# Optimization experiments

Measured on AMD Instinct MI355X. Metric: run time of the kernel, lower is better.

## Reference

```python
import jax, jax.numpy as jnp
import numpy as np

EMBEDDING_DIM = 64
N_EMBEDDINGS = 512


def setup_inputs() -> dict:
    key = jax.random.key(0)
    k1, k2 = jax.random.split(key)
    inputs = jax.random.normal(k1, (32, 64, 64, 64), dtype=jnp.float32)  # NCHW, C==embedding_dim
    weight = jax.random.normal(k2, (N_EMBEDDINGS, EMBEDDING_DIM), dtype=jnp.float32)
    return {"inputs": inputs, "weight": weight}


def reference(inputs, weight):
    # NCHW -> NHWC, flatten to [N, D]
    x = jnp.transpose(inputs, (0, 2, 3, 1))  # [B, H, W, D]
    in_shape = x.shape
    flat = x.reshape(-1, EMBEDDING_DIM)  # [N, D]

    distances = (
        jnp.sum(flat * flat, axis=1, keepdims=True)
        + jnp.sum(weight * weight, axis=1)
        - 2.0 * flat @ weight.T
    )
    idx = jnp.argmin(distances, axis=1)  # [N]

    # one-hot @ weight is just a gather
    quantized = weight[idx].reshape(in_shape)  # [B, H, W, D]

    # commitment loss: mse(stop_grad(quantized), x)
    e_latent_loss = jnp.mean(jnp.square(jax.lax.stop_gradient(quantized) - x))

    # straight-through estimator
    quantized = x + jax.lax.stop_gradient(quantized - x)

    return jnp.transpose(quantized, (0, 3, 1, 2)), e_latent_loss
```

## Files before the change

### kernel.cpp

```cpp
#include <hip/hip_runtime.h>
#include <math.h>

typedef short bf16x8 __attribute__((ext_vector_type(8)));
typedef float f32x4 __attribute__((ext_vector_type(4)));

#define VQ_D 64
#define VQ_K 512
#define VQ_NQ 131072
#define VQ_TOTAL 8388608
#define NT 32
#define TAU 8e-3f

__device__ __forceinline__ ushort bf16_rne(float f) {
    uint u = __builtin_bit_cast(uint, f);
    u += 0x7fffu + ((u >> 16) & 1u);
    return (ushort)(u >> 16);
}
__device__ __forceinline__ float bf16_to_f(ushort h) {
    uint u = ((uint)h) << 16;
    return __builtin_bit_cast(float, u);
}

__global__ __launch_bounds__(128) void vq_prep(const float* __restrict__ w,
                                               ushort* __restrict__ wfrag,
                                               float* __restrict__ wn,
                                               float* __restrict__ out) {
    if (blockIdx.x == 0 && threadIdx.x == 0) out[VQ_TOTAL] = 0.f;
    const int k = blockIdx.x * 128 + threadIdx.x;
    const float4* row = (const float4*)(w + k * VQ_D);
    const int t = k >> 4, col = k & 15;
    float nrm = 0.f;
    for (int g = 0; g < 8; ++g) {
        float4 a = row[2 * g], b4 = row[2 * g + 1];
        float v[8] = {a.x, a.y, a.z, a.w, b4.x, b4.y, b4.z, b4.w};
        ushort hi[8], lo[8];
#pragma unroll
        for (int j = 0; j < 8; ++j) {
            nrm = fmaf(v[j], v[j], nrm);
            hi[j] = bf16_rne(v[j]);
            lo[j] = bf16_rne(v[j] - bf16_to_f(hi[j]));
        }
        const int quad = g & 3, fh = g >> 2;
        const int lane = quad * 16 + col;
        bf16x8* basez = (bf16x8*)wfrag + t * 256 + lane;
        *(basez + fh * 64)       = *(bf16x8*)hi;
        *(basez + (2 + fh) * 64) = *(bf16x8*)lo;
    }
    wn[k] = nrm;
}

__global__ __launch_bounds__(256, 3) void vq_main(const float* __restrict__ in,
                                                  const float* __restrict__ w,
                                                  const ushort* __restrict__ wfrag,
                                                  const float* __restrict__ wng,
                                                  float* __restrict__ out) {
    __shared__ float xn_lds[128];
    __shared__ float best_lds[128], sec_lds[128];
    __shared__ int   bi_lds[128], si_lds[128];

    const int tid  = threadIdx.x;
    const int lane = tid & 63;
    const int wid  = tid >> 6;
    const int col  = lane & 15;
    const int quad = lane >> 4;
    const int n0  = blockIdx.x * 128;
    const int b   = n0 >> 12;
    const int hw0 = n0 & 4095;
    const float* xg0 = in + (b << 18) + hw0;
    const float* xgW = xg0 + wid * 32;

    bf16x8 ah0[2], ah1[2], al0[2], al1[2];
#pragma unroll
    for (int T = 0; T < 2; ++T) {
        const float* xq = xgW + T * 16 + col;
        float sx = 0.f;
        ushort h0[8], l0[8], h1[8], l1[8];
#pragma unroll
        for (int j = 0; j < 8; ++j) {
            float v0 = xq[(quad * 8 + j) << 12];
            float v1 = xq[(32 + quad * 8 + j) << 12];
            sx = fmaf(v0, v0, sx);
            sx = fmaf(v1, v1, sx);
            h0[j] = bf16_rne(v0); l0[j] = bf16_rne(v0 - bf16_to_f(h0[j]));
            h1[j] = bf16_rne(v1); l1[j] = bf16_rne(v1 - bf16_to_f(h1[j]));
        }
        ah0[T] = *(bf16x8*)h0; al0[T] = *(bf16x8*)l0;
        ah1[T] = *(bf16x8*)h1; al1[T] = *(bf16x8*)l1;
        sx += __shfl_xor(sx, 16, 64);
        sx += __shfl_xor(sx, 32, 64);
        if (quad == 0) xn_lds[wid * 32 + T * 16 + col] = sx;
    }

    float best[8], sec[8];
#pragma unroll
    for (int r = 0; r < 8; ++r) { best[r] = 3.0e38f; sec[r] = 3.0e38f; }

    const bf16x8* wf = (const bf16x8*)wfrag + lane;
    bf16x8 bh0 = wf[0], bh1 = wf[64], bl0 = wf[128], bl1 = wf[192];
    float wnv = wng[col];

#pragma unroll 1
    for (int t = 0; t < NT; ++t) {
        bf16x8 nh0, nh1, nl0, nl1;
        float wnn;
        if (t + 1 < NT) {
            const bf16x8* nx = wf + (t + 1) * 256;
            nh0 = nx[0]; nh1 = nx[64]; nl0 = nx[128]; nl1 = nx[192];
            wnn = wng[(t + 1) * 16 + col];
        }
#pragma unroll
        for (int T = 0; T < 2; ++T) {
            f32x4 accP = {0.f, 0.f, 0.f, 0.f}, accQ = {0.f, 0.f, 0.f, 0.f};
            accP = __builtin_amdgcn_mfma_f32_16x16x32_bf16(ah0[T], bh0, accP, 0, 0, 0);
            accP = __builtin_amdgcn_mfma_f32_16x16x32_bf16(ah1[T], bh1, accP, 0, 0, 0);
            accQ = __builtin_amdgcn_mfma_f32_16x16x32_bf16(ah0[T], bl0, accQ, 0, 0, 0);
            accQ = __builtin_amdgcn_mfma_f32_16x16x32_bf16(ah1[T], bl1, accQ, 0, 0, 0);
            accQ = __builtin_amdgcn_mfma_f32_16x16x32_bf16(al0[T], bh0, accQ, 0, 0, 0);
            accQ = __builtin_amdgcn_mfma_f32_16x16x32_bf16(al1[T], bh1, accQ, 0, 0, 0);
#pragma unroll
            for (int j = 0; j < 4; ++j) {
                float dist = fmaf(-2.f, accP[j] + accQ[j], wnv);
                uint u = (__builtin_bit_cast(uint, dist) & 0xFFFFFFE0u) | (uint)t;
                float key = __builtin_bit_cast(float, u);
                const int r = T * 4 + j;
                float m = fmaxf(best[r], key);
                best[r] = fminf(best[r], key);
                sec[r]  = fminf(sec[r], m);
            }
        }
        bh0 = nh0; bh1 = nh1; bl0 = nl0; bl1 = nl1; wnv = wnn;
    }

    float bD[8], sD[8];
    int bI[8], sI[8];
#pragma unroll
    for (int r = 0; r < 8; ++r) {
        uint ub = __builtin_bit_cast(uint, best[r]);
        uint us = __builtin_bit_cast(uint, sec[r]);
        bI[r] = (int)(ub & 31u) * 16 + col;
        sI[r] = (int)(us & 31u) * 16 + col;
        bD[r] = __builtin_bit_cast(float, ub & 0xFFFFFFE0u);
        sD[r] = __builtin_bit_cast(float, us & 0xFFFFFFE0u);
    }

#pragma unroll
    for (int off = 1; off < 16; off <<= 1) {
#pragma unroll
        for (int r = 0; r < 8; ++r) {
            float ob = __shfl_xor(bD[r], off, 64);
            float os = __shfl_xor(sD[r], off, 64);
            int   oi = __shfl_xor(bI[r], off, 64);
            int   oc = __shfl_xor(sI[r], off, 64);
            bool oWins = (ob < bD[r]) || (ob == bD[r] && oi < bI[r]);
            float nb  = oWins ? ob    : bD[r];
            int   ni  = oWins ? oi    : bI[r];
            float c1  = oWins ? bD[r] : ob;
            int   ci1 = oWins ? bI[r] : oi;
            float c2  = oWins ? os    : sD[r];
            int   ci2 = oWins ? oc    : sI[r];
            bool c1w = (c1 < c2) || (c1 == c2 && ci1 < ci2);
            sD[r] = c1w ? c1  : c2;
            sI[r] = c1w ? ci1 : ci2;
            bD[r] = nb; bI[r] = ni;
        }
    }
    if (col == 0) {
#pragma unroll
        for (int r = 0; r < 8; ++r) {
            const int q = wid * 32 + (r >> 2) * 16 + quad * 4 + (r & 3);
            best_lds[q] = bD[r]; sec_lds[q] = sD[r];
            bi_lds[q] = bI[r];   si_lds[q] = sI[r];
        }
    }
    __syncthreads();

    if (tid < 128) {
        const int q = tid;
        float cb = best_lds[q], cs = sec_lds[q];
        int cbi = bi_lds[q], csi = si_lds[q];
        double chosen = (double)cb;
        if (cs - cb < TAU) {
            const float* wb  = w + cbi * VQ_D;
            const float* ws2 = w + csi * VQ_D;
            const float* xqp = xg0 + q;
            double nb = 0.0, dotb = 0.0, ns = 0.0, dots = 0.0;
            for (int d = 0; d < VQ_D; ++d) {
                double xv = (double)xqp[d << 12];
                double wbv = (double)wb[d], wsv = (double)ws2[d];
                nb = fma(wbv, wbv, nb); dotb = fma(xv, wbv, dotb);
                ns = fma(wsv, wsv, ns); dots = fma(xv, wsv, dots);
            }
            double db = nb - 2.0 * dotb, ds = ns - 2.0 * dots;
            if (ds < db || (ds == db && csi < cbi)) { cbi = csi; chosen = ds; }
            else                                    { chosen = db; }
        }
        bi_lds[q] = cbi;
        double lq = (double)xn_lds[q] + chosen;
#pragma unroll
        for (int off = 32; off > 0; off >>= 1)
            lq += __shfl_down(lq, off, 64);
        if ((tid & 63) == 0)
            atomicAdd(out + VQ_TOTAL, (float)(lq * (1.0 / (double)VQ_TOTAL)));
    }
    __syncthreads();

    {
        const int q = tid & 127, half = tid >> 7;
        const float4* wrow = (const float4*)(w + bi_lds[q] * VQ_D) + half * 8;
        float* op = out + (b << 18) + hw0 + q;
#pragma unroll
        for (int u = 0; u < 8; ++u) {
            float4 v = wrow[u];
            const int d = half * 32 + 4 * u;
            op[(d + 0) << 12] = v.x;
            op[(d + 1) << 12] = v.y;
            op[(d + 2) << 12] = v.z;
            op[(d + 3) << 12] = v.w;
        }
    }
}

extern "C" void kernel_launch(void* const* d_in, const int* in_sizes, int n_in,
                              void* d_out, int out_size, void* d_ws, size_t ws_size,
                              hipStream_t stream) {
    const float* in = (const float*)d_in[0];
    const float* w  = (const float*)d_in[1];
    float* out = (float*)d_out;

    ushort* wfrag = (ushort*)d_ws;
    float*  wn    = (float*)((char*)d_ws + 131072);

    vq_prep<<<4, 128, 0, stream>>>(w, wfrag, wn, out);
    vq_main<<<VQ_NQ / 128, 256, 0, stream>>>(in, w, wfrag, wn, out);
}
```

Before: 139.7 us.

## Split codebook across two waves per 32-query block and merge top-2 in LDS

Each block now handles 32 queries with two waves, each scanning half of the codebook (16 tiles), and the two waves' best and second-best candidates are merged through LDS. The MFMA accumulators are merged into a single chain and the software prefetch of the next weight tile is removed. The aim is more blocks and waves for latency hiding and a shorter per-wave loop. In exchange, each input column is loaded twice (once per wave), atomics per query block rise fourfold, and the MFMA chain becomes serial with no prefetch.

After: 179.7 us. 1.29x slower.

```diff
diff --git a/kernel.cpp b/kernel.cpp
--- a/kernel.cpp
+++ b/kernel.cpp
@@ -8,7 +8,7 @@
 #define VQ_K 512
 #define VQ_NQ 131072
 #define VQ_TOTAL 8388608
-#define NT 32
+#define NTH 16
 #define TAU 8e-3f
 
 __device__ __forceinline__ ushort bf16_rne(float f) {
@@ -49,30 +49,29 @@
     wn[k] = nrm;
 }
 
-__global__ __launch_bounds__(256, 3) void vq_main(const float* __restrict__ in,
+__global__ __launch_bounds__(128, 6) void vq_main(const float* __restrict__ in,
                                                   const float* __restrict__ w,
                                                   const ushort* __restrict__ wfrag,
                                                   const float* __restrict__ wng,
                                                   float* __restrict__ out) {
-    __shared__ float xn_lds[128];
-    __shared__ float best_lds[128], sec_lds[128];
-    __shared__ int   bi_lds[128], si_lds[128];
+    __shared__ uint4 mrg_lds[2][32];
+    __shared__ float xn_lds[32];
+    __shared__ int   bi_lds[32];
 
     const int tid  = threadIdx.x;
     const int lane = tid & 63;
-    const int wid  = tid >> 6;
+    const int half = tid >> 6;
     const int col  = lane & 15;
     const int quad = lane >> 4;
-    const int n0  = blockIdx.x * 128;
+    const int n0  = blockIdx.x * 32;
     const int b   = n0 >> 12;
     const int hw0 = n0 & 4095;
     const float* xg0 = in + (b << 18) + hw0;
-    const float* xgW = xg0 + wid * 32;
 
     bf16x8 ah0[2], ah1[2], al0[2], al1[2];
 #pragma unroll
     for (int T = 0; T < 2; ++T) {
-        const float* xq = xgW + T * 16 + col;
+        const float* xq = xg0 + T * 16 + col;
         float sx = 0.f;
         ushort h0[8], l0[8], h1[8], l1[8];
 #pragma unroll
@@ -88,39 +87,34 @@
         ah1[T] = *(bf16x8*)h1; al1[T] = *(bf16x8*)l1;
         sx += __shfl_xor(sx, 16, 64);
         sx += __shfl_xor(sx, 32, 64);
-        if (quad == 0) xn_lds[wid * 32 + T * 16 + col] = sx;
+        if (quad == 0 && half == 0) xn_lds[T * 16 + col] = sx;
     }
 
     float best[8], sec[8];
 #pragma unroll
     for (int r = 0; r < 8; ++r) { best[r] = 3.0e38f; sec[r] = 3.0e38f; }
 
-    const bf16x8* wf = (const bf16x8*)wfrag + lane;
-    bf16x8 bh0 = wf[0], bh1 = wf[64], bl0 = wf[128], bl1 = wf[192];
-    float wnv = wng[col];
+    const bf16x8* wfb = (const bf16x8*)wfrag + lane + half * (NTH * 256);
 
 #pragma unroll 1
-    for (int t = 0; t < NT; ++t) {
-        bf16x8 nh0, nh1, nl0, nl1;
-        float wnn;
-        if (t + 1 < NT) {
-            const bf16x8* nx = wf + (t + 1) * 256;
-            nh0 = nx[0]; nh1 = nx[64]; nl0 = nx[128]; nl1 = nx[192];
-            wnn = wng[(t + 1) * 16 + col];
-        }
+    for (int tl = 0; tl < NTH; ++tl) {
+        const int tg = half * NTH + tl;
+        const bf16x8* wf = wfb + tl * 256;
+        const bf16x8 bh0 = wf[0], bh1 = wf[64], bl0 = wf[128], bl1 = wf[192];
+        const float wnv = wng[tg * 16 + col];
 #pragma unroll
         for (int T = 0; T < 2; ++T) {
-            f32x4 accP = {0.f, 0.f, 0.f, 0.f}, accQ = {0.f, 0.f, 0.f, 0.f};
-            accP = __builtin_amdgcn_mfma_f32_16x16x32_bf16(ah0[T], bh0, accP, 0, 0, 0);
-            accP = __builtin_amdgcn_mfma_f32_16x16x32_bf16(ah1[T], bh1, accP, 0, 0, 0);
-            accQ = __builtin_amdgcn_mfma_f32_16x16x32_bf16(ah0[T], bl0, accQ, 0, 0, 0);
-            accQ = __builtin_amdgcn_mfma_f32_16x16x32_bf16(ah1[T], bl1, accQ, 0, 0, 0);
-            accQ = __builtin_amdgcn_mfma_f32_16x16x32_bf16(al0[T], bh0, accQ, 0, 0, 0);
-            accQ = __builtin_amdgcn_mfma_f32_16x16x32_bf16(al1[T], bh1, accQ, 0, 0, 0);
+            f32x4 acc = {0.f, 0.f, 0.f, 0.f};
+            acc = __builtin_amdgcn_mfma_f32_16x16x32_bf16(ah0[T], bh0, acc, 0, 0, 0);
+            acc = __builtin_amdgcn_mfma_f32_16x16x32_bf16(ah1[T], bh1, acc, 0, 0, 0);
+            acc = __builtin_amdgcn_mfma_f32_16x16x32_bf16(ah0[T], bl0, acc, 0, 0, 0);
+            acc = __builtin_amdgcn_mfma_f32_16x16x32_bf16(ah1[T], bl1, acc, 0, 0, 0);
+            acc = __builtin_amdgcn_mfma_f32_16x16x32_bf16(al0[T], bh0, acc, 0, 0, 0);
+            acc = __builtin_amdgcn_mfma_f32_16x16x32_bf16(al1[T], bh1, acc, 0, 0, 0);
 #pragma unroll
             for (int j = 0; j < 4; ++j) {
-                float dist = fmaf(-2.f, accP[j] + accQ[j], wnv);
-                uint u = (__builtin_bit_cast(uint, dist) & 0xFFFFFFE0u) | (uint)t;
+                float dist = fmaf(-2.f, acc[j], wnv);
+                uint u = (__builtin_bit_cast(uint, dist) & 0xFFFFFFE0u) | (uint)tg;
                 float key = __builtin_bit_cast(float, u);
                 const int r = T * 4 + j;
                 float m = fmaxf(best[r], key);
@@ -128,7 +122,6 @@
                 sec[r]  = fminf(sec[r], m);
             }
         }
-        bh0 = nh0; bh1 = nh1; bl0 = nl0; bl1 = nl1; wnv = wnn;
     }
 
     float bD[8], sD[8];
@@ -167,51 +160,66 @@
     if (col == 0) {
 #pragma unroll
         for (int r = 0; r < 8; ++r) {
-            const int q = wid * 32 + (r >> 2) * 16 + quad * 4 + (r & 3);
-            best_lds[q] = bD[r]; sec_lds[q] = sD[r];
-            bi_lds[q] = bI[r];   si_lds[q] = sI[r];
+            const int q = (r >> 2) * 16 + quad * 4 + (r & 3);
+            mrg_lds[half][q] = make_uint4(__builtin_bit_cast(uint, bD[r]), (uint)bI[r],
+                                          __builtin_bit_cast(uint, sD[r]), (uint)sI[r]);
         }
     }
     __syncthreads();
 
-    if (tid < 128) {
-        const int q = tid;
-        float cb = best_lds[q], cs = sec_lds[q];
-        int cbi = bi_lds[q], csi = si_lds[q];
-        double chosen = (double)cb;
-        if (cs - cb < TAU) {
-            const float* wb  = w + cbi * VQ_D;
-            const float* ws2 = w + csi * VQ_D;
-            const float* xqp = xg0 + q;
-            double nb = 0.0, dotb = 0.0, ns = 0.0, dots = 0.0;
-            for (int d = 0; d < VQ_D; ++d) {
-                double xv = (double)xqp[d << 12];
-                double wbv = (double)wb[d], wsv = (double)ws2[d];
-                nb = fma(wbv, wbv, nb); dotb = fma(xv, wbv, dotb);
-                ns = fma(wsv, wsv, ns); dots = fma(xv, wsv, dots);
+    if (half == 0) {
+        const int q = lane;
+        float cb = 0.f, cs = 0.f;
+        int cbi = 0, csi = 0;
+        double lq = 0.0;
+        if (lane < 32) {
+            uint4 A = mrg_lds[0][q], B = mrg_lds[1][q];
+            float da = __builtin_bit_cast(float, A.x), db_ = __builtin_bit_cast(float, B.x);
+            float sa = __builtin_bit_cast(float, A.z), sb = __builtin_bit_cast(float, B.z);
+            int ia = (int)A.y, ib = (int)B.y, ja = (int)A.w, jb = (int)B.w;
+            bool aw = (da < db_) || (da == db_ && ia < ib);
+            cb  = aw ? da : db_;  cbi = aw ? ia : ib;
+            float c1  = aw ? db_ : da;  int ci1 = aw ? ib : ia;
+            float c2  = aw ? sa  : sb;  int ci2 = aw ? ja : jb;
+            bool c1w = (c1 < c2) || (c1 == c2 && ci1 < ci2);
+            cs  = c1w ? c1  : c2;
+            csi = c1w ? ci1 : ci2;
+
+            double chosen = (double)cb;
+            if (cs - cb < TAU) {
+                const float* wb  = w + cbi * VQ_D;
+                const float* ws2 = w + csi * VQ_D;
+                const float* xqp = xg0 + q;
+                double nb = 0.0, dotb = 0.0, ns = 0.0, dots = 0.0;
+                for (int d = 0; d < VQ_D; ++d) {
+                    double xv = (double)xqp[d << 12];
+                    double wbv = (double)wb[d], wsv = (double)ws2[d];
+                    nb = fma(wbv, wbv, nb); dotb = fma(xv, wbv, dotb);
+                    ns = fma(wsv, wsv, ns); dots = fma(xv, wsv, dots);
+                }
+                double db2 = nb - 2.0 * dotb, ds2 = ns - 2.0 * dots;
+                if (ds2 < db2 || (ds2 == db2 && csi < cbi)) { cbi = csi; chosen = ds2; }
+                else                                        { chosen = db2; }
             }
-            double db = nb - 2.0 * dotb, ds = ns - 2.0 * dots;
-            if (ds < db || (ds == db && csi < cbi)) { cbi = csi; chosen = ds; }
-            else                                    { chosen = db; }
-        }
-        bi_lds[q] = cbi;
-        double lq = (double)xn_lds[q] + chosen;
+            bi_lds[q] = cbi;
+            lq = (double)xn_lds[q] + chosen;
+        }
 #pragma unroll
         for (int off = 32; off > 0; off >>= 1)
             lq += __shfl_down(lq, off, 64);
-        if ((tid & 63) == 0)
+        if (lane == 0)
             atomicAdd(out + VQ_TOTAL, (float)(lq * (1.0 / (double)VQ_TOTAL)));
     }
     __syncthreads();
 
     {
-        const int q = tid & 127, half = tid >> 7;
-        const float4* wrow = (const float4*)(w + bi_lds[q] * VQ_D) + half * 8;
+        const int q = tid & 31, u4 = tid >> 5;
+        const float4* wrow = (const float4*)(w + bi_lds[q] * VQ_D) + u4 * 4;
         float* op = out + (b << 18) + hw0 + q;
 #pragma unroll
-        for (int u = 0; u < 8; ++u) {
+        for (int u = 0; u < 4; ++u) {
             float4 v = wrow[u];
-            const int d = half * 32 + 4 * u;
+            const int d = u4 * 16 + 4 * u;
             op[(d + 0) << 12] = v.x;
             op[(d + 1) << 12] = v.y;
             op[(d + 2) << 12] = v.z;
@@ -231,5 +239,5 @@
     float*  wn    = (float*)((char*)d_ws + 131072);
 
     vq_prep<<<4, 128, 0, stream>>>(w, wfrag, wn, out);
-    vq_main<<<VQ_NQ / 128, 256, 0, stream>>>(in, w, wfrag, wn, out);
-}
+    vq_main<<<VQ_NQ / 32, 128, 0, stream>>>(in, w, wfrag, wn, out);
+}
```
